# Optimization experiments

Hardware: AMD Instinct MI355X
Metric: run time of the kernel (lower is better)

The kernel has to match this reference:

```python
import jax, jax.numpy as jnp
import numpy as np

N_NODES = 50000
N_EDGES = 1600000
IN_DIM, HIDDEN, OUT_DIM = 128, 128, 64


def setup_inputs() -> dict:
    key = jax.random.key(0)
    ks = jax.random.split(key, 8)
    x = jax.random.normal(ks[0], (N_NODES, IN_DIM), dtype=jnp.float32)
    edge_index = jax.random.randint(ks[1], (2, N_EDGES), 0, N_NODES, dtype=jnp.int64)
    # SAGEConv params: lin_l applied to aggregated neighbors (with bias),
    # lin_r applied to root/self features (no bias) -- PyG defaults.
    def lin_init(k, fan_in, fan_out):
        bound = 1.0 / np.sqrt(fan_in)
        return jax.random.uniform(k, (fan_in, fan_out), jnp.float32, -bound, bound)
    W1_l = lin_init(ks[2], IN_DIM, HIDDEN)
    W1_r = lin_init(ks[3], IN_DIM, HIDDEN)
    b1 = jnp.zeros((HIDDEN,), jnp.float32)
    W2_l = lin_init(ks[4], HIDDEN, OUT_DIM)
    W2_r = lin_init(ks[5], HIDDEN, OUT_DIM)
    b2 = jnp.zeros((OUT_DIM,), jnp.float32)
    return {"x": x, "edge_index": edge_index, "W1_l": W1_l, "W1_r": W1_r,
            "b1": b1, "W2_l": W2_l, "W2_r": W2_r, "b2": b2}


def _sage_conv(h, src, dst, n_nodes, W_l, W_r, b):
    # gather messages from source nodes, mean-aggregate at destinations
    msg = h[src]                                              # [E, D]
    agg_sum = jax.ops.segment_sum(msg, dst, num_segments=n_nodes)
    deg = jax.ops.segment_sum(jnp.ones((src.shape[0],), h.dtype), dst,
                              num_segments=n_nodes)
    agg_mean = agg_sum / jnp.maximum(deg, 1.0)[:, None]       # [N, D]
    return agg_mean @ W_l + h @ W_r + b


def reference(x, edge_index, W1_l, W1_r, b1, W2_l, W2_r, b2):
    n = x.shape[0]
    src, dst = edge_index[0], edge_index[1]
    h = jax.nn.relu(_sage_conv(x, src, dst, n, W1_l, W1_r, b1))
    return _sage_conv(h, src, dst, n, W2_l, W2_r, b2)
```

## Files before the change

### kernel.cpp

```cpp
#include <hip/hip_runtime.h>

#define NN 50000
#define NE 1600000
#define BSTRIDE 96
#define BNODES 25
#define C_BKT 2000
#define P1_BLKS 256
#define P1_CHUNK 6250
#define ZID 50000
#define XCVT_BLKS 1563
#define WCVT_BLKS 48
#define PP_PREP (XCVT_BLKS + WCVT_BLKS)
#define RGRP 3128

typedef __bf16 bf16x8 __attribute__((ext_vector_type(8)));
typedef float  f32x4  __attribute__((ext_vector_type(4)));
typedef float  f32x2  __attribute__((ext_vector_type(2)));

__device__ __forceinline__ float bfLo(uint u) { union { uint i; float f; } v; v.i = u << 16; return v.f; }
__device__ __forceinline__ float bfHi(uint u) { union { uint i; float f; } v; v.i = u & 0xffff0000u; return v.f; }
__device__ __forceinline__ f32x2 bfPair(uint u) {
    union { uint i[2]; f32x2 f; } v; v.i[0] = u << 16; v.i[1] = u & 0xffff0000u; return v.f;
}
__device__ __forceinline__ ushort f2bf(float f) {
    union { float f; uint i; } v; v.f = f;
    uint r = v.i + 0x7fffu + ((v.i >> 16) & 1u);
    return (ushort)(r >> 16);
}
__device__ __forceinline__ uint pack2(float a, float b) {
    return (uint)f2bf(a) | ((uint)f2bf(b) << 16);
}
__device__ __forceinline__ bf16x8 load8(const ushort* p) {
    union { uint4 u; bf16x8 b; } v; v.u = *(const uint4*)p; return v.b;
}

#define ACC8P(u) { b0 += bfPair(u.x); b1 += bfPair(u.y); b2 += bfPair(u.z); b3 += bfPair(u.w); }

#define CVA(u, o) { f32x2 p0 = __builtin_amdgcn_cvt_pk_f32_fp8((int)(u), 0); \
                    f32x2 p1 = __builtin_amdgcn_cvt_pk_f32_fp8((int)(u), 1); \
                    a[(o)] += p0; a[(o)+1] += p1; }
#define ACCF8(v) { CVA((v).x, 0); CVA((v).y, 2); CVA((v).z, 4); CVA((v).w, 6); }

__device__ __forceinline__ int pkOff(int n, int k) {
    return (((n >> 4) * 4 + (k >> 5)) * 512) + (((k >> 3) & 3) * 128) + ((n & 15) * 8) + (k & 7);
}

__global__ __launch_bounds__(1024) void k_pp(
    const float4* __restrict__ x, ushort* __restrict__ xbp, uint* __restrict__ xf8,
    const float* __restrict__ W1l, const float* __restrict__ W1r,
    const float* __restrict__ W2l, const float* __restrict__ W2r,
    ushort* __restrict__ T1l, ushort* __restrict__ T1r,
    ushort* __restrict__ T2l, ushort* __restrict__ T2r,
    const int* __restrict__ src, const int* __restrict__ dst,
    uint* __restrict__ cells, uint* __restrict__ offc, ushort* __restrict__ hW) {
    __shared__ uint hist[C_BKT + 1];
    __shared__ uint part[250];
    const int b = blockIdx.x;
    const int tid = threadIdx.x;
    if (b < XCVT_BLKS) {
        int i = b * 1024 + tid;
        if (i < NN * 128 / 4) {
            float4 v = x[i];
            int r = i >> 5, k0 = (i & 31) * 4;
            ushort4 o; o.x = f2bf(v.x); o.y = f2bf(v.y); o.z = f2bf(v.z); o.w = f2bf(v.w);
            *(ushort4*)(xbp + pkOff(r, k0)) = o;
            uint rr = (uint)__builtin_amdgcn_cvt_pk_fp8_f32(v.x, v.y, 0, 0);
            rr = (uint)__builtin_amdgcn_cvt_pk_fp8_f32(v.z, v.w, (int)rr, 1);
            xf8[i] = rr;
        } else if (b == XCVT_BLKS - 1) {
            if (tid >= 512 && tid < 544) xf8[(size_t)ZID * 32 + (tid - 512)] = 0;
            else if (tid >= 544 && tid < 576) ((uint*)hW)[(size_t)ZID * 32 + (tid - 544)] = 0;
        }
    } else if (b < PP_PREP) {
        int i = (b - XCVT_BLKS) * 1024 + tid;
        if (i < 16384) {
            int k = i >> 7, n = i & 127; T1l[pkOff(n, k)] = f2bf(W1l[i]);
        } else if (i < 32768) {
            int j = i - 16384; int k = j >> 7, n = j & 127; T1r[pkOff(n, k)] = f2bf(W1r[j]);
        } else if (i < 40960) {
            int j = i - 32768; int k = j >> 6, n = j & 63;  T2l[pkOff(n, k)] = f2bf(W2l[j]);
        } else {
            int j = i - 40960; int k = j >> 6, n = j & 63;  T2r[pkOff(n, k)] = f2bf(W2r[j]);
        }
    } else {
        const int b2 = b - PP_PREP;
        for (int i = tid; i < C_BKT; i += 1024) hist[i] = 0;
        __syncthreads();
        const int beg = b2 * P1_CHUNK;
        for (int i = beg + tid; i < beg + P1_CHUNK; i += 1024)
            atomicAdd(&hist[dst[i] / BNODES], 1);
        __syncthreads();
        if (tid < 250) {
            uint s = 0;
            #pragma unroll
            for (int k = 0; k < 8; k++) {
                uint t = hist[tid * 8 + k];
                hist[tid * 8 + k] = s;
                s += t;
            }
            part[tid] = s;
        }
        __syncthreads();
        if (tid == 0) {
            uint run = 0;
            for (int t = 0; t < 250; t++) { uint tmp = part[t]; part[t] = run; run += tmp; }
        }
        __syncthreads();
        if (tid < 250) {
            uint bs = part[tid];
            if (bs) {
                #pragma unroll
                for (int k = 0; k < 8; k++) hist[tid * 8 + k] += bs;
            }
        }
        __syncthreads();
        for (int c = tid; c < C_BKT; c += 1024) {
            uint st = hist[c];
            uint en = (c == C_BKT - 1) ? (uint)P1_CHUNK : hist[c + 1];
            offc[(size_t)c * P1_BLKS + b2] = st | ((en - st) << 16);
        }
        __syncthreads();
        uint* myCells = cells + (size_t)b2 * P1_CHUNK;
        for (int i = beg + tid; i < beg + P1_CHUNK; i += 1024) {
            int d = dst[i];
            int s = src[i];
            int c = d / BNODES;
            uint p = atomicAdd(&hist[c], 1);
            myCells[p] = ((uint)(d - c * BNODES) << 16) | (uint)s;
        }
    }
}

__global__ __launch_bounds__(256) void k_pagg(
    const uint* __restrict__ cells, const uint* __restrict__ offc,
    const uchar* __restrict__ xf8, ushort* __restrict__ col,
    int* __restrict__ deg, ushort* __restrict__ aggp) {
    __shared__ uint hist[BNODES];
    __shared__ __align__(16) ushort colS[BNODES * BSTRIDE];
    const int bid = blockIdx.x;
    const int c = (bid & 7) * 250 + (bid >> 3);
    const int tid = threadIdx.x;
    if (tid < BNODES) hist[tid] = 0;
    __syncthreads();
    {
        uint v = offc[(size_t)c * P1_BLKS + tid];
        int st = (int)(v & 0xFFFF), n = (int)(v >> 16);
        const uint* cell = cells + (size_t)tid * P1_CHUNK + st;
        for (int j = 0; j < n; j++) {
            uint e = cell[j];
            int dl = e >> 16;
            uint p = atomicAdd(&hist[dl], 1);
            if (p < BSTRIDE) colS[dl * BSTRIDE + p] = (ushort)(e & 0xFFFF);
        }
    }
    __syncthreads();
    const int nodeBase = c * BNODES;
    if (tid < BNODES) {
        deg[nodeBase + tid] = (int)hist[tid];
        int dd = min((int)hist[tid], BSTRIDE);
        int dr = (dd + 7) & ~7;
        for (int j = dd; j < dr; j++) colS[tid * BSTRIDE + j] = (ushort)ZID;
    }
    __syncthreads();
    {
        uint4* cg = (uint4*)(col + (size_t)nodeBase * BSTRIDE);
        const uint4* cs = (const uint4*)colS;
        for (int i = tid; i < BNODES * BSTRIDE / 8; i += 256) cg[i] = cs[i];
    }
    const int wave = tid >> 6, lane = tid & 63;
    const int q = lane >> 3;
    const int cc = lane & 7;
    for (int ln = wave; ln < BNODES; ln += 4) {
        int d = (int)hist[ln];
        int dd = min(d, BSTRIDE);
        int nb = ((dd + 7) & ~7) >> 3;
        const int base = ln * BSTRIDE;
        f32x2 a[8];
        #pragma unroll
        for (int i = 0; i < 8; i++) a[i] = (f32x2){0.f, 0.f};
        int t = 0;
        for (; t + 4 <= nb; t += 4) {
            int s0 = (int)colS[base + t * 8 + q];
            int s1 = (int)colS[base + t * 8 + 8 + q];
            int s2 = (int)colS[base + t * 8 + 16 + q];
            int s3 = (int)colS[base + t * 8 + 24 + q];
            uint4 u0 = *(const uint4*)(xf8 + (size_t)s0 * 128 + cc * 16);
            uint4 u1 = *(const uint4*)(xf8 + (size_t)s1 * 128 + cc * 16);
            uint4 u2 = *(const uint4*)(xf8 + (size_t)s2 * 128 + cc * 16);
            uint4 u3 = *(const uint4*)(xf8 + (size_t)s3 * 128 + cc * 16);
            ACCF8(u0); ACCF8(u1); ACCF8(u2); ACCF8(u3);
        }
        for (; t < nb; t++) {
            int s = (int)colS[base + t * 8 + q];
            uint4 u = *(const uint4*)(xf8 + (size_t)s * 128 + cc * 16);
            ACCF8(u);
        }
        #pragma unroll
        for (int m = 8; m < 64; m <<= 1) {
            #pragma unroll
            for (int i = 0; i < 8; i++) {
                f32x2 t2;
                t2.x = __shfl_xor(a[i].x, m);
                t2.y = __shfl_xor(a[i].y, m);
                a[i] += t2;
            }
        }
        if (q == 0) {
            int node = nodeBase + ln;
            float inv = 1.f / fmaxf((float)d, 1.f);
            #pragma unroll
            for (int i = 0; i < 8; i++) a[i] *= inv;
            int basep = ((node >> 4) * 4 + (cc >> 1)) * 512 + ((cc & 1) * 2) * 128 + (node & 15) * 8;
            uint4 o;
            o.x = pack2(a[0].x, a[0].y);
            o.y = pack2(a[1].x, a[1].y);
            o.z = pack2(a[2].x, a[2].y);
            o.w = pack2(a[3].x, a[3].y);
            *(uint4*)(aggp + basep) = o;
            o.x = pack2(a[4].x, a[4].y);
            o.y = pack2(a[5].x, a[5].y);
            o.z = pack2(a[6].x, a[6].y);
            o.w = pack2(a[7].x, a[7].y);
            *(uint4*)(aggp + basep + 128) = o;
        }
    }
}

#define PAD1 136
__global__ __launch_bounds__(256) void k_gemm12(
    const ushort* __restrict__ aggp, const ushort* __restrict__ xbp,
    const ushort* __restrict__ T1l, const ushort* __restrict__ T1r,
    const ushort* __restrict__ T2l, const ushort* __restrict__ T2r,
    const float* __restrict__ b1, const float* __restrict__ b2,
    ushort* __restrict__ hW, float* __restrict__ outp) {
    __shared__ ushort hS[2][16 * PAD1];
    const int lane = threadIdx.x & 63;
    const int wave = threadIdx.x >> 6;
    const int s = wave >> 1;
    const int ch = wave & 1;
    const int quad = lane >> 4, r16 = lane & 15;
    const int row0 = blockIdx.x * 32 + s * 16;
    const int g = blockIdx.x * 2 + s;
    ushort* myS = &hS[s][0];

    f32x4 acc[4];
    #pragma unroll
    for (int nt = 0; nt < 4; nt++) acc[nt] = (f32x4){0.f, 0.f, 0.f, 0.f};
    #pragma unroll
    for (int kt = 0; kt < 4; kt++) {
        bf16x8 aAgg = load8(aggp + (size_t)(g * 4 + kt) * 512 + lane * 8);
        bf16x8 aXb  = load8(xbp  + (size_t)(g * 4 + kt) * 512 + lane * 8);
        #pragma unroll
        for (int nt = 0; nt < 4; nt++) {
            const int tile = ((ch * 4 + nt) * 4 + kt) * 512 + lane * 8;
            acc[nt] = __builtin_amdgcn_mfma_f32_16x16x32_bf16(aAgg, load8(T1l + tile), acc[nt], 0, 0, 0);
            acc[nt] = __builtin_amdgcn_mfma_f32_16x16x32_bf16(aXb,  load8(T1r + tile), acc[nt], 0, 0, 0);
        }
    }
    #pragma unroll
    for (int nt = 0; nt < 4; nt++) {
        int cc = ch * 64 + nt * 16 + r16;
        float bv = b1[cc];
        #pragma unroll
        for (int i = 0; i < 4; i++)
            myS[(quad * 4 + i) * PAD1 + cc] = f2bf(fmaxf(acc[nt][i] + bv, 0.f));
    }
    __syncthreads();

    f32x4 acc2[2], acc3[2];
    #pragma unroll
    for (int nt = 0; nt < 2; nt++) {
        acc2[nt] = (f32x4){0.f, 0.f, 0.f, 0.f};
        acc3[nt] = (f32x4){0.f, 0.f, 0.f, 0.f};
    }
    #pragma unroll
    for (int kt = 0; kt < 4; kt++) {
        bf16x8 ah = load8(&myS[r16 * PAD1 + kt * 32 + quad * 8]);
        #pragma unroll
        for (int nt = 0; nt < 2; nt++) {
            const int tile = ((ch * 2 + nt) * 4 + kt) * 512 + lane * 8;
            acc2[nt] = __builtin_amdgcn_mfma_f32_16x16x32_bf16(ah, load8(T2l + tile), acc2[nt], 0, 0, 0);
            acc3[nt] = __builtin_amdgcn_mfma_f32_16x16x32_bf16(ah, load8(T2r + tile), acc3[nt], 0, 0, 0);
        }
    }
    #pragma unroll
    for (int nt = 0; nt < 2; nt++) {
        int cc = ch * 32 + nt * 16 + r16;
        float bv = b2[cc];
        #pragma unroll
        for (int i = 0; i < 4; i++) {
            int rr = row0 + quad * 4 + i;
            if (rr < NN) {
                hW[(size_t)rr * 64 + cc] = f2bf(acc2[nt][i]);
                outp[(size_t)rr * 64 + cc] = acc3[nt][i] + bv;
            }
        }
    }
}

__global__ __launch_bounds__(256) void k_agg64f(
    const ushort* __restrict__ hW, const ushort* __restrict__ col,
    const int* __restrict__ deg, const float* __restrict__ outp,
    float* __restrict__ out) {
    __shared__ __align__(16) ushort colB[4 * BSTRIDE];
    const int tid = threadIdx.x;
    const int node0 = blockIdx.x * 4;
    if (tid < 48) {
        const uint4* cg = (const uint4*)(col + (size_t)node0 * BSTRIDE);
        *(uint4*)&colB[tid * 8] = cg[tid];
    }
    __syncthreads();
    const int wave = tid >> 6, lane = tid & 63;
    const int node = node0 + wave;
    const int q = lane >> 3;
    const int c = lane & 7;
    const int base = wave * BSTRIDE;
    int d = deg[node];
    int dd = min(d, BSTRIDE);
    int nb = ((dd + 7) & ~7) >> 3;
    f32x2 b0 = {0.f,0.f}, b1 = {0.f,0.f}, b2 = {0.f,0.f}, b3 = {0.f,0.f};
    int t = 0;
    for (; t + 4 <= nb; t += 4) {
        int s0 = (int)colB[base + t * 8 + q];
        int s1 = (int)colB[base + t * 8 + 8 + q];
        int s2 = (int)colB[base + t * 8 + 16 + q];
        int s3 = (int)colB[base + t * 8 + 24 + q];
        uint4 u0 = *(const uint4*)(hW + (size_t)s0 * 64 + c * 8);
        uint4 u1 = *(const uint4*)(hW + (size_t)s1 * 64 + c * 8);
        uint4 u2 = *(const uint4*)(hW + (size_t)s2 * 64 + c * 8);
        uint4 u3 = *(const uint4*)(hW + (size_t)s3 * 64 + c * 8);
        ACC8P(u0); ACC8P(u1); ACC8P(u2); ACC8P(u3);
    }
    for (; t < nb; t++) {
        int s = (int)colB[base + t * 8 + q];
        uint4 u = *(const uint4*)(hW + (size_t)s * 64 + c * 8);
        ACC8P(u);
    }
    #pragma unroll
    for (int m = 8; m < 64; m <<= 1) {
        f32x2 t0, t1, t2, t3;
        t0.x = __shfl_xor(b0.x, m); t0.y = __shfl_xor(b0.y, m);
        t1.x = __shfl_xor(b1.x, m); t1.y = __shfl_xor(b1.y, m);
        t2.x = __shfl_xor(b2.x, m); t2.y = __shfl_xor(b2.y, m);
        t3.x = __shfl_xor(b3.x, m); t3.y = __shfl_xor(b3.y, m);
        b0 += t0; b1 += t1; b2 += t2; b3 += t3;
    }
    if (q == 0) {
        float inv = 1.f / fmaxf((float)d, 1.f);
        float4 p0 = *(const float4*)(outp + (size_t)node * 64 + c * 8);
        float4 p1 = *(const float4*)(outp + (size_t)node * 64 + c * 8 + 4);
        float4 o;
        o.x = b0.x * inv + p0.x; o.y = b0.y * inv + p0.y;
        o.z = b1.x * inv + p0.z; o.w = b1.y * inv + p0.w;
        *(float4*)(out + (size_t)node * 64 + c * 8) = o;
        o.x = b2.x * inv + p1.x; o.y = b2.y * inv + p1.y;
        o.z = b3.x * inv + p1.z; o.w = b3.y * inv + p1.w;
        *(float4*)(out + (size_t)node * 64 + c * 8 + 4) = o;
    }
}

extern "C" void kernel_launch(void* const* d_in, const int* in_sizes, int n_in,
                              void* d_out, int out_size, void* d_ws, size_t ws_size,
                              hipStream_t stream) {
    const float* x   = (const float*)d_in[0];
    const int*   ei  = (const int*)d_in[1];
    const float* W1l = (const float*)d_in[2];
    const float* W1r = (const float*)d_in[3];
    const float* b1  = (const float*)d_in[4];
    const float* W2l = (const float*)d_in[5];
    const float* W2r = (const float*)d_in[6];
    const float* b2  = (const float*)d_in[7];
    float* out = (float*)d_out;

    const int* src = ei;
    const int* dst = ei + NE;

    char* w = (char*)d_ws;
    ushort* col   = (ushort*)w;                  w += (size_t)NN * BSTRIDE * 2;
    int* deg      = (int*)w;                     w += (size_t)50048 * 4;
    uint* offc    = (uint*)w;                    w += (size_t)C_BKT * P1_BLKS * 4;
    ushort* xbp   = (ushort*)w;                  w += (size_t)RGRP * 2048 * 2;
    ushort* T1l   = (ushort*)w;                  w += 128 * 128 * 2;
    ushort* T1r   = (ushort*)w;                  w += 128 * 128 * 2;
    ushort* T2l   = (ushort*)w;                  w += 64 * 128 * 2;
    ushort* T2r   = (ushort*)w;                  w += 64 * 128 * 2;
    ushort* aggp  = (ushort*)w;                  w += (size_t)RGRP * 2048 * 2;
    ushort* hW    = (ushort*)w;                  w += (size_t)(NN + 16) * 64 * 2;
    float* outp   = (float*)w;                   w += (size_t)NN * 64 * 4;
    uchar* xf8    = (uchar*)w;                   w += (size_t)(NN + 16) * 128;
    uint* cells   = (uint*)w;                    w += (size_t)NE * 4;

    k_pp<<<PP_PREP + P1_BLKS, 1024, 0, stream>>>(
        (const float4*)x, xbp, (uint*)xf8, W1l, W1r, W2l, W2r,
        T1l, T1r, T2l, T2r, src, dst, cells, offc, hW);

    k_pagg<<<C_BKT, 256, 0, stream>>>(cells, offc, xf8, col, deg, aggp);

    k_gemm12<<<(NN + 31) / 32, 256, 0, stream>>>(aggp, xbp, T1l, T1r, T2l, T2r, b1, b2, hW, outp);

    k_agg64f<<<NN / 4, 256, 0, stream>>>(hW, col, deg, outp, out);
}
```

Baseline: 201.9 us.

## Split gathered feature tables into column halves to shrink per-pass working set

The fp8 input features and the bf16 layer-2 hidden features are stored as two separate column-half arrays. Both aggregation kernels launch twice as many blocks, and each block gathers only one half, with 16 edges in flight per wave instead of 8. The aim is to halve the random-gather working set per block so it fits the L2/MALL caches better, and to raise parallelism. In exchange, the edge bucketing and the column-list scan in k_pagg are repeated for both halves, and padding rounds to 16.

```diff
diff --git a/kernel.cpp b/kernel.cpp
--- a/kernel.cpp
+++ b/kernel.cpp
@@ -17,8 +17,6 @@
 typedef float  f32x4  __attribute__((ext_vector_type(4)));
 typedef float  f32x2  __attribute__((ext_vector_type(2)));
 
-__device__ __forceinline__ float bfLo(uint u) { union { uint i; float f; } v; v.i = u << 16; return v.f; }
-__device__ __forceinline__ float bfHi(uint u) { union { uint i; float f; } v; v.i = u & 0xffff0000u; return v.f; }
 __device__ __forceinline__ f32x2 bfPair(uint u) {
     union { uint i[2]; f32x2 f; } v; v.i[0] = u << 16; v.i[1] = u & 0xffff0000u; return v.f;
 }
@@ -46,13 +44,15 @@
 }
 
 __global__ __launch_bounds__(1024) void k_pp(
-    const float4* __restrict__ x, ushort* __restrict__ xbp, uint* __restrict__ xf8,
+    const float4* __restrict__ x, ushort* __restrict__ xbp,
+    uint* __restrict__ xf8lo, uint* __restrict__ xf8hi,
     const float* __restrict__ W1l, const float* __restrict__ W1r,
     const float* __restrict__ W2l, const float* __restrict__ W2r,
     ushort* __restrict__ T1l, ushort* __restrict__ T1r,
     ushort* __restrict__ T2l, ushort* __restrict__ T2r,
     const int* __restrict__ src, const int* __restrict__ dst,
-    uint* __restrict__ cells, uint* __restrict__ offc, ushort* __restrict__ hW) {
+    uint* __restrict__ cells, uint* __restrict__ offc,
+    uint* __restrict__ hWlo, uint* __restrict__ hWhi) {
     __shared__ uint hist[C_BKT + 1];
     __shared__ uint part[250];
     const int b = blockIdx.x;
@@ -61,15 +61,18 @@
         int i = b * 1024 + tid;
         if (i < NN * 128 / 4) {
             float4 v = x[i];
-            int r = i >> 5, k0 = (i & 31) * 4;
+            int r = i >> 5, j = i & 31;
             ushort4 o; o.x = f2bf(v.x); o.y = f2bf(v.y); o.z = f2bf(v.z); o.w = f2bf(v.w);
-            *(ushort4*)(xbp + pkOff(r, k0)) = o;
+            *(ushort4*)(xbp + pkOff(r, j * 4)) = o;
             uint rr = (uint)__builtin_amdgcn_cvt_pk_fp8_f32(v.x, v.y, 0, 0);
             rr = (uint)__builtin_amdgcn_cvt_pk_fp8_f32(v.z, v.w, (int)rr, 1);
-            xf8[i] = rr;
+            uint* pl = (j < 16) ? xf8lo : xf8hi;
+            pl[(size_t)r * 16 + (j & 15)] = rr;
         } else if (b == XCVT_BLKS - 1) {
-            if (tid >= 512 && tid < 544) xf8[(size_t)ZID * 32 + (tid - 512)] = 0;
-            else if (tid >= 544 && tid < 576) ((uint*)hW)[(size_t)ZID * 32 + (tid - 544)] = 0;
+            if (tid >= 512 && tid < 528) xf8lo[(size_t)ZID * 16 + (tid - 512)] = 0;
+            else if (tid >= 528 && tid < 544) xf8hi[(size_t)ZID * 16 + (tid - 528)] = 0;
+            else if (tid >= 544 && tid < 560) hWlo[(size_t)ZID * 16 + (tid - 544)] = 0;
+            else if (tid >= 560 && tid < 576) hWhi[(size_t)ZID * 16 + (tid - 560)] = 0;
         }
     } else if (b < PP_PREP) {
         int i = (b - XCVT_BLKS) * 1024 + tid;
@@ -133,13 +136,15 @@
 
 __global__ __launch_bounds__(256) void k_pagg(
     const uint* __restrict__ cells, const uint* __restrict__ offc,
-    const uchar* __restrict__ xf8, ushort* __restrict__ col,
-    int* __restrict__ deg, ushort* __restrict__ aggp) {
+    const uchar* __restrict__ xf8lo, const uchar* __restrict__ xf8hi,
+    ushort* __restrict__ col, int* __restrict__ deg, ushort* __restrict__ aggp) {
     __shared__ uint hist[BNODES];
     __shared__ __align__(16) ushort colS[BNODES * BSTRIDE];
     const int bid = blockIdx.x;
-    const int c = (bid & 7) * 250 + (bid >> 3);
+    const int h = bid & 1;
+    const int c = ((bid >> 1) & 3) * 500 + (bid >> 3);
     const int tid = threadIdx.x;
+    const uchar* xf8 = h ? xf8hi : xf8lo;
     if (tid < BNODES) hist[tid] = 0;
     __syncthreads();
     {
@@ -156,47 +161,43 @@
     __syncthreads();
     const int nodeBase = c * BNODES;
     if (tid < BNODES) {
-        deg[nodeBase + tid] = (int)hist[tid];
+        if (h == 0) deg[nodeBase + tid] = (int)hist[tid];
         int dd = min((int)hist[tid], BSTRIDE);
-        int dr = (dd + 7) & ~7;
+        int dr = (dd + 15) & ~15;
         for (int j = dd; j < dr; j++) colS[tid * BSTRIDE + j] = (ushort)ZID;
     }
     __syncthreads();
-    {
+    if (h == 0) {
         uint4* cg = (uint4*)(col + (size_t)nodeBase * BSTRIDE);
         const uint4* cs = (const uint4*)colS;
         for (int i = tid; i < BNODES * BSTRIDE / 8; i += 256) cg[i] = cs[i];
     }
     const int wave = tid >> 6, lane = tid & 63;
-    const int q = lane >> 3;
-    const int cc = lane & 7;
+    const int q = lane >> 2;
+    const int c4 = lane & 3;
     for (int ln = wave; ln < BNODES; ln += 4) {
         int d = (int)hist[ln];
         int dd = min(d, BSTRIDE);
-        int nb = ((dd + 7) & ~7) >> 3;
+        int nb = ((dd + 15) & ~15) >> 4;
         const int base = ln * BSTRIDE;
         f32x2 a[8];
         #pragma unroll
         for (int i = 0; i < 8; i++) a[i] = (f32x2){0.f, 0.f};
         int t = 0;
-        for (; t + 4 <= nb; t += 4) {
-            int s0 = (int)colS[base + t * 8 + q];
-            int s1 = (int)colS[base + t * 8 + 8 + q];
-            int s2 = (int)colS[base + t * 8 + 16 + q];
-            int s3 = (int)colS[base + t * 8 + 24 + q];
-            uint4 u0 = *(const uint4*)(xf8 + (size_t)s0 * 128 + cc * 16);
-            uint4 u1 = *(const uint4*)(xf8 + (size_t)s1 * 128 + cc * 16);
-            uint4 u2 = *(const uint4*)(xf8 + (size_t)s2 * 128 + cc * 16);
-            uint4 u3 = *(const uint4*)(xf8 + (size_t)s3 * 128 + cc * 16);
-            ACCF8(u0); ACCF8(u1); ACCF8(u2); ACCF8(u3);
+        for (; t + 2 <= nb; t += 2) {
+            int s0 = (int)colS[base + t * 16 + q];
+            int s1 = (int)colS[base + t * 16 + 16 + q];
+            uint4 u0 = *(const uint4*)(xf8 + (size_t)s0 * 64 + c4 * 16);
+            uint4 u1 = *(const uint4*)(xf8 + (size_t)s1 * 64 + c4 * 16);
+            ACCF8(u0); ACCF8(u1);
         }
         for (; t < nb; t++) {
-            int s = (int)colS[base + t * 8 + q];
-            uint4 u = *(const uint4*)(xf8 + (size_t)s * 128 + cc * 16);
+            int s = (int)colS[base + t * 16 + q];
+            uint4 u = *(const uint4*)(xf8 + (size_t)s * 64 + c4 * 16);
             ACCF8(u);
         }
         #pragma unroll
-        for (int m = 8; m < 64; m <<= 1) {
+        for (int m = 4; m < 64; m <<= 1) {
             #pragma unroll
             for (int i = 0; i < 8; i++) {
                 f32x2 t2;
@@ -210,7 +211,8 @@
             float inv = 1.f / fmaxf((float)d, 1.f);
             #pragma unroll
             for (int i = 0; i < 8; i++) a[i] *= inv;
-            int basep = ((node >> 4) * 4 + (cc >> 1)) * 512 + ((cc & 1) * 2) * 128 + (node & 15) * 8;
+            int kt = h * 2 + (c4 >> 1);
+            int basep = ((node >> 4) * 4 + kt) * 512 + ((c4 & 1) * 2) * 128 + (node & 15) * 8;
             uint4 o;
             o.x = pack2(a[0].x, a[0].y);
             o.y = pack2(a[1].x, a[1].y);
@@ -232,7 +234,7 @@
     const ushort* __restrict__ T1l, const ushort* __restrict__ T1r,
     const ushort* __restrict__ T2l, const ushort* __restrict__ T2r,
     const float* __restrict__ b1, const float* __restrict__ b2,
-    ushort* __restrict__ hW, float* __restrict__ outp) {
+    ushort* __restrict__ hWlo, ushort* __restrict__ hWhi, float* __restrict__ outp) {
     __shared__ ushort hS[2][16 * PAD1];
     const int lane = threadIdx.x & 63;
     const int wave = threadIdx.x >> 6;
@@ -283,6 +285,7 @@
             acc3[nt] = __builtin_amdgcn_mfma_f32_16x16x32_bf16(ah, load8(T2r + tile), acc3[nt], 0, 0, 0);
         }
     }
+    ushort* hWp = ch ? hWhi : hWlo;
     #pragma unroll
     for (int nt = 0; nt < 2; nt++) {
         int cc = ch * 32 + nt * 16 + r16;
@@ -291,7 +294,7 @@
         for (int i = 0; i < 4; i++) {
             int rr = row0 + quad * 4 + i;
             if (rr < NN) {
-                hW[(size_t)rr * 64 + cc] = f2bf(acc2[nt][i]);
+                hWp[(size_t)rr * 32 + nt * 16 + r16] = f2bf(acc2[nt][i]);
                 outp[(size_t)rr * 64 + cc] = acc3[nt][i] + bv;
             }
         }
@@ -299,45 +302,44 @@
 }
 
 __global__ __launch_bounds__(256) void k_agg64f(
-    const ushort* __restrict__ hW, const ushort* __restrict__ col,
-    const int* __restrict__ deg, const float* __restrict__ outp,
-    float* __restrict__ out) {
+    const ushort* __restrict__ hWlo, const ushort* __restrict__ hWhi,
+    const ushort* __restrict__ col, const int* __restrict__ deg,
+    const float* __restrict__ outp, float* __restrict__ out) {
     __shared__ __align__(16) ushort colB[4 * BSTRIDE];
+    const int bid = blockIdx.x;
+    const int h = bid & 1;
+    const int node0 = (bid >> 1) * 4;
     const int tid = threadIdx.x;
-    const int node0 = blockIdx.x * 4;
     if (tid < 48) {
         const uint4* cg = (const uint4*)(col + (size_t)node0 * BSTRIDE);
         *(uint4*)&colB[tid * 8] = cg[tid];
     }
     __syncthreads();
+    const ushort* hw = h ? hWhi : hWlo;
     const int wave = tid >> 6, lane = tid & 63;
     const int node = node0 + wave;
-    const int q = lane >> 3;
-    const int c = lane & 7;
+    const int q = lane >> 2;
+    const int c4 = lane & 3;
     const int base = wave * BSTRIDE;
     int d = deg[node];
     int dd = min(d, BSTRIDE);
-    int nb = ((dd + 7) & ~7) >> 3;
+    int nb = ((dd + 15) & ~15) >> 4;
     f32x2 b0 = {0.f,0.f}, b1 = {0.f,0.f}, b2 = {0.f,0.f}, b3 = {0.f,0.f};
     int t = 0;
-    for (; t + 4 <= nb; t += 4) {
-        int s0 = (int)colB[base + t * 8 + q];
-        int s1 = (int)colB[base + t * 8 + 8 + q];
-        int s2 = (int)colB[base + t * 8 + 16 + q];
-        int s3 = (int)colB[base + t * 8 + 24 + q];
-        uint4 u0 = *(const uint4*)(hW + (size_t)s0 * 64 + c * 8);
-        uint4 u1 = *(const uint4*)(hW + (size_t)s1 * 64 + c * 8);
-        uint4 u2 = *(const uint4*)(hW + (size_t)s2 * 64 + c * 8);
-        uint4 u3 = *(const uint4*)(hW + (size_t)s3 * 64 + c * 8);
-        ACC8P(u0); ACC8P(u1); ACC8P(u2); ACC8P(u3);
+    for (; t + 2 <= nb; t += 2) {
+        int s0 = (int)colB[base + t * 16 + q];
+        int s1 = (int)colB[base + t * 16 + 16 + q];
+        uint4 u0 = *(const uint4*)(hw + (size_t)s0 * 32 + c4 * 8);
+        uint4 u1 = *(const uint4*)(hw + (size_t)s1 * 32 + c4 * 8);
+        ACC8P(u0); ACC8P(u1);
     }
     for (; t < nb; t++) {
-        int s = (int)colB[base + t * 8 + q];
-        uint4 u = *(const uint4*)(hW + (size_t)s * 64 + c * 8);
+        int s = (int)colB[base + t * 16 + q];
+        uint4 u = *(const uint4*)(hw + (size_t)s * 32 + c4 * 8);
         ACC8P(u);
     }
     #pragma unroll
-    for (int m = 8; m < 64; m <<= 1) {
+    for (int m = 4; m < 64; m <<= 1) {
         f32x2 t0, t1, t2, t3;
         t0.x = __shfl_xor(b0.x, m); t0.y = __shfl_xor(b0.y, m);
         t1.x = __shfl_xor(b1.x, m); t1.y = __shfl_xor(b1.y, m);
@@ -347,15 +349,16 @@
     }
     if (q == 0) {
         float inv = 1.f / fmaxf((float)d, 1.f);
-        float4 p0 = *(const float4*)(outp + (size_t)node * 64 + c * 8);
-        float4 p1 = *(const float4*)(outp + (size_t)node * 64 + c * 8 + 4);
+        size_t o0 = (size_t)node * 64 + h * 32 + c4 * 8;
+        float4 p0 = *(const float4*)(outp + o0);
+        float4 p1 = *(const float4*)(outp + o0 + 4);
         float4 o;
         o.x = b0.x * inv + p0.x; o.y = b0.y * inv + p0.y;
         o.z = b1.x * inv + p0.z; o.w = b1.y * inv + p0.w;
-        *(float4*)(out + (size_t)node * 64 + c * 8) = o;
+        *(float4*)(out + o0) = o;
         o.x = b2.x * inv + p1.x; o.y = b2.y * inv + p1.y;
         o.z = b3.x * inv + p1.z; o.w = b3.y * inv + p1.w;
-        *(float4*)(out + (size_t)node * 64 + c * 8 + 4) = o;
+        *(float4*)(out + o0 + 4) = o;
     }
 }
 
@@ -385,18 +388,20 @@
     ushort* T2l   = (ushort*)w;                  w += 64 * 128 * 2;
     ushort* T2r   = (ushort*)w;                  w += 64 * 128 * 2;
     ushort* aggp  = (ushort*)w;                  w += (size_t)RGRP * 2048 * 2;
-    ushort* hW    = (ushort*)w;                  w += (size_t)(NN + 16) * 64 * 2;
+    ushort* hWlo  = (ushort*)w;                  w += (size_t)(NN + 16) * 32 * 2;
+    ushort* hWhi  = (ushort*)w;                  w += (size_t)(NN + 16) * 32 * 2;
     float* outp   = (float*)w;                   w += (size_t)NN * 64 * 4;
-    uchar* xf8    = (uchar*)w;                   w += (size_t)(NN + 16) * 128;
+    uchar* xf8lo  = (uchar*)w;                   w += (size_t)(NN + 16) * 64;
+    uchar* xf8hi  = (uchar*)w;                   w += (size_t)(NN + 16) * 64;
     uint* cells   = (uint*)w;                    w += (size_t)NE * 4;
 
     k_pp<<<PP_PREP + P1_BLKS, 1024, 0, stream>>>(
-        (const float4*)x, xbp, (uint*)xf8, W1l, W1r, W2l, W2r,
-        T1l, T1r, T2l, T2r, src, dst, cells, offc, hW);
-
-    k_pagg<<<C_BKT, 256, 0, stream>>>(cells, offc, xf8, col, deg, aggp);
-
-    k_gemm12<<<(NN + 31) / 32, 256, 0, stream>>>(aggp, xbp, T1l, T1r, T2l, T2r, b1, b2, hW, outp);
-
-    k_agg64f<<<NN / 4, 256, 0, stream>>>(hW, col, deg, outp, out);
-}
+        (const float4*)x, xbp, (uint*)xf8lo, (uint*)xf8hi, W1l, W1r, W2l, W2r,
+        T1l, T1r, T2l, T2r, src, dst, cells, offc, (uint*)hWlo, (uint*)hWhi);
+
+    k_pagg<<<C_BKT * 2, 256, 0, stream>>>(cells, offc, xf8lo, xf8hi, col, deg, aggp);
+
+    k_gemm12<<<(NN + 31) / 32, 256, 0, stream>>>(aggp, xbp, T1l, T1r, T2l, T2r, b1, b2, hWlo, hWhi, outp);
+
+    k_agg64f<<<(NN / 4) * 2, 256, 0, stream>>>(hWlo, hWhi, col, deg, outp, out);
+}
```

Result: slower. 258.8 us (+28.2%).

## Replace two-pass bucketed CSR build with direct global-atomic scatter into padded adjacency

Applied to the files above, without the earlier changes.

Drops the per-block shared-memory histogram, prefix scan and bucketed cells staging. Each edge now takes a slot with a global atomicAdd on a per-node counter and writes its source straight into the fixed-stride column array. This needs a separate zeroing kernel, and the counters double as degrees. The layer-1 aggregation now reads the prebuilt columns per node and handles the partial last group by masking lanes to the zero row instead of padding. This removes a full extra pass over the edges, but adds contention from 1.6M global atomics and scattered 2-byte writes, and the neighbor order within each node becomes nondeterministic.

```diff
diff --git a/kernel.cpp b/kernel.cpp
--- a/kernel.cpp
+++ b/kernel.cpp
@@ -3,11 +3,9 @@
 #define NN 50000
 #define NE 1600000
 #define BSTRIDE 96
-#define BNODES 25
-#define C_BKT 2000
-#define P1_BLKS 256
-#define P1_CHUNK 6250
 #define ZID 50000
+#define SCAT_BLKS 256
+#define SCHUNK 6250
 #define XCVT_BLKS 1563
 #define WCVT_BLKS 48
 #define PP_PREP (XCVT_BLKS + WCVT_BLKS)
@@ -17,8 +15,6 @@
 typedef float  f32x4  __attribute__((ext_vector_type(4)));
 typedef float  f32x2  __attribute__((ext_vector_type(2)));
 
-__device__ __forceinline__ float bfLo(uint u) { union { uint i; float f; } v; v.i = u << 16; return v.f; }
-__device__ __forceinline__ float bfHi(uint u) { union { uint i; float f; } v; v.i = u & 0xffff0000u; return v.f; }
 __device__ __forceinline__ f32x2 bfPair(uint u) {
     union { uint i[2]; f32x2 f; } v; v.i[0] = u << 16; v.i[1] = u & 0xffff0000u; return v.f;
 }
@@ -43,6 +39,11 @@
 
 __device__ __forceinline__ int pkOff(int n, int k) {
     return (((n >> 4) * 4 + (k >> 5)) * 512) + (((k >> 3) & 3) * 128) + ((n & 15) * 8) + (k & 7);
+}
+
+__global__ __launch_bounds__(256) void k_zero(int* __restrict__ cur) {
+    int i = blockIdx.x * 256 + threadIdx.x;
+    if (i < NN) cur[i] = 0;
 }
 
 __global__ __launch_bounds__(1024) void k_pp(
@@ -52,18 +53,16 @@
     ushort* __restrict__ T1l, ushort* __restrict__ T1r,
     ushort* __restrict__ T2l, ushort* __restrict__ T2r,
     const int* __restrict__ src, const int* __restrict__ dst,
-    uint* __restrict__ cells, uint* __restrict__ offc, ushort* __restrict__ hW) {
-    __shared__ uint hist[C_BKT + 1];
-    __shared__ uint part[250];
+    int* __restrict__ cur, ushort* __restrict__ col, ushort* __restrict__ hW) {
     const int b = blockIdx.x;
     const int tid = threadIdx.x;
     if (b < XCVT_BLKS) {
         int i = b * 1024 + tid;
         if (i < NN * 128 / 4) {
             float4 v = x[i];
-            int r = i >> 5, k0 = (i & 31) * 4;
+            int r = i >> 5, j = i & 31;
             ushort4 o; o.x = f2bf(v.x); o.y = f2bf(v.y); o.z = f2bf(v.z); o.w = f2bf(v.w);
-            *(ushort4*)(xbp + pkOff(r, k0)) = o;
+            *(ushort4*)(xbp + pkOff(r, j * 4)) = o;
             uint rr = (uint)__builtin_amdgcn_cvt_pk_fp8_f32(v.x, v.y, 0, 0);
             rr = (uint)__builtin_amdgcn_cvt_pk_fp8_f32(v.z, v.w, (int)rr, 1);
             xf8[i] = rr;
@@ -84,145 +83,88 @@
         }
     } else {
         const int b2 = b - PP_PREP;
-        for (int i = tid; i < C_BKT; i += 1024) hist[i] = 0;
-        __syncthreads();
-        const int beg = b2 * P1_CHUNK;
-        for (int i = beg + tid; i < beg + P1_CHUNK; i += 1024)
-            atomicAdd(&hist[dst[i] / BNODES], 1);
-        __syncthreads();
-        if (tid < 250) {
-            uint s = 0;
-            #pragma unroll
-            for (int k = 0; k < 8; k++) {
-                uint t = hist[tid * 8 + k];
-                hist[tid * 8 + k] = s;
-                s += t;
-            }
-            part[tid] = s;
-        }
-        __syncthreads();
-        if (tid == 0) {
-            uint run = 0;
-            for (int t = 0; t < 250; t++) { uint tmp = part[t]; part[t] = run; run += tmp; }
-        }
-        __syncthreads();
-        if (tid < 250) {
-            uint bs = part[tid];
-            if (bs) {
-                #pragma unroll
-                for (int k = 0; k < 8; k++) hist[tid * 8 + k] += bs;
-            }
-        }
-        __syncthreads();
-        for (int c = tid; c < C_BKT; c += 1024) {
-            uint st = hist[c];
-            uint en = (c == C_BKT - 1) ? (uint)P1_CHUNK : hist[c + 1];
-            offc[(size_t)c * P1_BLKS + b2] = st | ((en - st) << 16);
-        }
-        __syncthreads();
-        uint* myCells = cells + (size_t)b2 * P1_CHUNK;
-        for (int i = beg + tid; i < beg + P1_CHUNK; i += 1024) {
+        const int beg = b2 * SCHUNK;
+        for (int i = beg + tid; i < beg + SCHUNK; i += 1024) {
             int d = dst[i];
             int s = src[i];
-            int c = d / BNODES;
-            uint p = atomicAdd(&hist[c], 1);
-            myCells[p] = ((uint)(d - c * BNODES) << 16) | (uint)s;
+            uint p = (uint)atomicAdd(&cur[d], 1);
+            if (p < BSTRIDE) col[(size_t)d * BSTRIDE + p] = (ushort)s;
         }
     }
 }
 
 __global__ __launch_bounds__(256) void k_pagg(
-    const uint* __restrict__ cells, const uint* __restrict__ offc,
-    const uchar* __restrict__ xf8, ushort* __restrict__ col,
-    int* __restrict__ deg, ushort* __restrict__ aggp) {
-    __shared__ uint hist[BNODES];
-    __shared__ __align__(16) ushort colS[BNODES * BSTRIDE];
-    const int bid = blockIdx.x;
-    const int c = (bid & 7) * 250 + (bid >> 3);
+    const uchar* __restrict__ xf8, const ushort* __restrict__ col,
+    const int* __restrict__ deg, ushort* __restrict__ aggp) {
+    __shared__ __align__(16) ushort colB[4 * BSTRIDE];
     const int tid = threadIdx.x;
-    if (tid < BNODES) hist[tid] = 0;
+    const int node0 = blockIdx.x * 4;
+    if (tid < 48) {
+        const uint4* cg = (const uint4*)(col + (size_t)node0 * BSTRIDE);
+        *(uint4*)&colB[tid * 8] = cg[tid];
+    }
     __syncthreads();
-    {
-        uint v = offc[(size_t)c * P1_BLKS + tid];
-        int st = (int)(v & 0xFFFF), n = (int)(v >> 16);
-        const uint* cell = cells + (size_t)tid * P1_CHUNK + st;
-        for (int j = 0; j < n; j++) {
-            uint e = cell[j];
-            int dl = e >> 16;
-            uint p = atomicAdd(&hist[dl], 1);
-            if (p < BSTRIDE) colS[dl * BSTRIDE + p] = (ushort)(e & 0xFFFF);
-        }
-    }
-    __syncthreads();
-    const int nodeBase = c * BNODES;
-    if (tid < BNODES) {
-        deg[nodeBase + tid] = (int)hist[tid];
-        int dd = min((int)hist[tid], BSTRIDE);
-        int dr = (dd + 7) & ~7;
-        for (int j = dd; j < dr; j++) colS[tid * BSTRIDE + j] = (ushort)ZID;
-    }
-    __syncthreads();
-    {
-        uint4* cg = (uint4*)(col + (size_t)nodeBase * BSTRIDE);
-        const uint4* cs = (const uint4*)colS;
-        for (int i = tid; i < BNODES * BSTRIDE / 8; i += 256) cg[i] = cs[i];
-    }
     const int wave = tid >> 6, lane = tid & 63;
+    const int node = node0 + wave;
     const int q = lane >> 3;
-    const int cc = lane & 7;
-    for (int ln = wave; ln < BNODES; ln += 4) {
-        int d = (int)hist[ln];
-        int dd = min(d, BSTRIDE);
-        int nb = ((dd + 7) & ~7) >> 3;
-        const int base = ln * BSTRIDE;
-        f32x2 a[8];
-        #pragma unroll
-        for (int i = 0; i < 8; i++) a[i] = (f32x2){0.f, 0.f};
-        int t = 0;
-        for (; t + 4 <= nb; t += 4) {
-            int s0 = (int)colS[base + t * 8 + q];
-            int s1 = (int)colS[base + t * 8 + 8 + q];
-            int s2 = (int)colS[base + t * 8 + 16 + q];
-            int s3 = (int)colS[base + t * 8 + 24 + q];
-            uint4 u0 = *(const uint4*)(xf8 + (size_t)s0 * 128 + cc * 16);
-            uint4 u1 = *(const uint4*)(xf8 + (size_t)s1 * 128 + cc * 16);
-            uint4 u2 = *(const uint4*)(xf8 + (size_t)s2 * 128 + cc * 16);
-            uint4 u3 = *(const uint4*)(xf8 + (size_t)s3 * 128 + cc * 16);
-            ACCF8(u0); ACCF8(u1); ACCF8(u2); ACCF8(u3);
-        }
-        for (; t < nb; t++) {
-            int s = (int)colS[base + t * 8 + q];
-            uint4 u = *(const uint4*)(xf8 + (size_t)s * 128 + cc * 16);
-            ACCF8(u);
-        }
-        #pragma unroll
-        for (int m = 8; m < 64; m <<= 1) {
-            #pragma unroll
-            for (int i = 0; i < 8; i++) {
-                f32x2 t2;
-                t2.x = __shfl_xor(a[i].x, m);
-                t2.y = __shfl_xor(a[i].y, m);
-                a[i] += t2;
-            }
-        }
-        if (q == 0) {
-            int node = nodeBase + ln;
-            float inv = 1.f / fmaxf((float)d, 1.f);
-            #pragma unroll
-            for (int i = 0; i < 8; i++) a[i] *= inv;
-            int basep = ((node >> 4) * 4 + (cc >> 1)) * 512 + ((cc & 1) * 2) * 128 + (node & 15) * 8;
-            uint4 o;
-            o.x = pack2(a[0].x, a[0].y);
-            o.y = pack2(a[1].x, a[1].y);
-            o.z = pack2(a[2].x, a[2].y);
-            o.w = pack2(a[3].x, a[3].y);
-            *(uint4*)(aggp + basep) = o;
-            o.x = pack2(a[4].x, a[4].y);
-            o.y = pack2(a[5].x, a[5].y);
-            o.z = pack2(a[6].x, a[6].y);
-            o.w = pack2(a[7].x, a[7].y);
-            *(uint4*)(aggp + basep + 128) = o;
-        }
+    const int c = lane & 7;
+    const int base = wave * BSTRIDE;
+    int d = deg[node];
+    int dd = min(d, BSTRIDE);
+    int nf = dd >> 3;
+    int rem = dd & 7;
+    f32x2 a[8];
+    #pragma unroll
+    for (int i = 0; i < 8; i++) a[i] = (f32x2){0.f, 0.f};
+    int t = 0;
+    for (; t + 4 <= nf; t += 4) {
+        int s0 = (int)colB[base + t * 8 + q];
+        int s1 = (int)colB[base + t * 8 + 8 + q];
+        int s2 = (int)colB[base + t * 8 + 16 + q];
+        int s3 = (int)colB[base + t * 8 + 24 + q];
+        uint4 u0 = *(const uint4*)(xf8 + (size_t)s0 * 128 + c * 16);
+        uint4 u1 = *(const uint4*)(xf8 + (size_t)s1 * 128 + c * 16);
+        uint4 u2 = *(const uint4*)(xf8 + (size_t)s2 * 128 + c * 16);
+        uint4 u3 = *(const uint4*)(xf8 + (size_t)s3 * 128 + c * 16);
+        ACCF8(u0); ACCF8(u1); ACCF8(u2); ACCF8(u3);
+    }
+    for (; t < nf; t++) {
+        int s = (int)colB[base + t * 8 + q];
+        uint4 u = *(const uint4*)(xf8 + (size_t)s * 128 + c * 16);
+        ACCF8(u);
+    }
+    if (rem) {
+        int slot = nf * 8 + q;
+        int s = (slot < dd) ? (int)colB[base + slot] : ZID;
+        uint4 u = *(const uint4*)(xf8 + (size_t)s * 128 + c * 16);
+        ACCF8(u);
+    }
+    #pragma unroll
+    for (int m = 8; m < 64; m <<= 1) {
+        #pragma unroll
+        for (int i = 0; i < 8; i++) {
+            f32x2 t2;
+            t2.x = __shfl_xor(a[i].x, m);
+            t2.y = __shfl_xor(a[i].y, m);
+            a[i] += t2;
+        }
+    }
+    if (q == 0) {
+        float inv = 1.f / fmaxf((float)d, 1.f);
+        #pragma unroll
+        for (int i = 0; i < 8; i++) a[i] *= inv;
+        int basep = ((node >> 4) * 4 + (c >> 1)) * 512 + ((c & 1) * 2) * 128 + (node & 15) * 8;
+        uint4 o;
+        o.x = pack2(a[0].x, a[0].y);
+        o.y = pack2(a[1].x, a[1].y);
+        o.z = pack2(a[2].x, a[2].y);
+        o.w = pack2(a[3].x, a[3].y);
+        *(uint4*)(aggp + basep) = o;
+        o.x = pack2(a[4].x, a[4].y);
+        o.y = pack2(a[5].x, a[5].y);
+        o.z = pack2(a[6].x, a[6].y);
+        o.w = pack2(a[7].x, a[7].y);
+        *(uint4*)(aggp + basep + 128) = o;
     }
 }
 
@@ -317,10 +259,11 @@
     const int base = wave * BSTRIDE;
     int d = deg[node];
     int dd = min(d, BSTRIDE);
-    int nb = ((dd + 7) & ~7) >> 3;
+    int nf = dd >> 3;
+    int rem = dd & 7;
     f32x2 b0 = {0.f,0.f}, b1 = {0.f,0.f}, b2 = {0.f,0.f}, b3 = {0.f,0.f};
     int t = 0;
-    for (; t + 4 <= nb; t += 4) {
+    for (; t + 4 <= nf; t += 4) {
         int s0 = (int)colB[base + t * 8 + q];
         int s1 = (int)colB[base + t * 8 + 8 + q];
         int s2 = (int)colB[base + t * 8 + 16 + q];
@@ -331,8 +274,14 @@
         uint4 u3 = *(const uint4*)(hW + (size_t)s3 * 64 + c * 8);
         ACC8P(u0); ACC8P(u1); ACC8P(u2); ACC8P(u3);
     }
-    for (; t < nb; t++) {
+    for (; t < nf; t++) {
         int s = (int)colB[base + t * 8 + q];
+        uint4 u = *(const uint4*)(hW + (size_t)s * 64 + c * 8);
+        ACC8P(u);
+    }
+    if (rem) {
+        int slot = nf * 8 + q;
+        int s = (slot < dd) ? (int)colB[base + slot] : ZID;
         uint4 u = *(const uint4*)(hW + (size_t)s * 64 + c * 8);
         ACC8P(u);
     }
@@ -377,8 +326,7 @@
 
     char* w = (char*)d_ws;
     ushort* col   = (ushort*)w;                  w += (size_t)NN * BSTRIDE * 2;
-    int* deg      = (int*)w;                     w += (size_t)50048 * 4;
-    uint* offc    = (uint*)w;                    w += (size_t)C_BKT * P1_BLKS * 4;
+    int* cur      = (int*)w;                     w += (size_t)50048 * 4;
     ushort* xbp   = (ushort*)w;                  w += (size_t)RGRP * 2048 * 2;
     ushort* T1l   = (ushort*)w;                  w += 128 * 128 * 2;
     ushort* T1r   = (ushort*)w;                  w += 128 * 128 * 2;
@@ -388,15 +336,16 @@
     ushort* hW    = (ushort*)w;                  w += (size_t)(NN + 16) * 64 * 2;
     float* outp   = (float*)w;                   w += (size_t)NN * 64 * 4;
     uchar* xf8    = (uchar*)w;                   w += (size_t)(NN + 16) * 128;
-    uint* cells   = (uint*)w;                    w += (size_t)NE * 4;
-
-    k_pp<<<PP_PREP + P1_BLKS, 1024, 0, stream>>>(
+
+    k_zero<<<(NN + 255) / 256, 256, 0, stream>>>(cur);
+
+    k_pp<<<PP_PREP + SCAT_BLKS, 1024, 0, stream>>>(
         (const float4*)x, xbp, (uint*)xf8, W1l, W1r, W2l, W2r,
-        T1l, T1r, T2l, T2r, src, dst, cells, offc, hW);
-
-    k_pagg<<<C_BKT, 256, 0, stream>>>(cells, offc, xf8, col, deg, aggp);
+        T1l, T1r, T2l, T2r, src, dst, cur, col, hW);
+
+    k_pagg<<<NN / 4, 256, 0, stream>>>(xf8, col, cur, aggp);
 
     k_gemm12<<<(NN + 31) / 32, 256, 0, stream>>>(aggp, xbp, T1l, T1r, T2l, T2r, b1, b2, hW, outp);
 
-    k_agg64f<<<NN / 4, 256, 0, stream>>>(hW, col, deg, outp, out);
-}
+    k_agg64f<<<NN / 4, 256, 0, stream>>>(hW, col, cur, outp, out);
+}
```

After: 279.3 us. +38.3%, slower.

## Split bucket slotting from first-layer gather into separate kernels

Applied to the files above, without the earlier changes.

The fused kernel that built each bucket's neighbor lists and then gathered FP8 features is split in two. The new k_slot kernel handles only slotting, with 50-node buckets, 512 threads and two threads per partition. A new k_gath1 kernel then aggregates one node per wave across many small blocks, and both gathers handle the partial last group of 8 neighbors with a masked load instead of relying on padding. This is meant to raise parallelism and balance load in the first aggregation, at the cost of an extra launch and a round trip of the col array through global memory.

```diff
diff --git a/kernel.cpp b/kernel.cpp
--- a/kernel.cpp
+++ b/kernel.cpp
@@ -3,8 +3,8 @@
 #define NN 50000
 #define NE 1600000
 #define BSTRIDE 96
-#define BNODES 25
-#define C_BKT 2000
+#define BNODES 50
+#define C_BKT 1000
 #define P1_BLKS 256
 #define P1_CHUNK 6250
 #define ZID 50000
@@ -17,8 +17,6 @@
 typedef float  f32x4  __attribute__((ext_vector_type(4)));
 typedef float  f32x2  __attribute__((ext_vector_type(2)));
 
-__device__ __forceinline__ float bfLo(uint u) { union { uint i; float f; } v; v.i = u << 16; return v.f; }
-__device__ __forceinline__ float bfHi(uint u) { union { uint i; float f; } v; v.i = u & 0xffff0000u; return v.f; }
 __device__ __forceinline__ f32x2 bfPair(uint u) {
     union { uint i[2]; f32x2 f; } v; v.i[0] = u << 16; v.i[1] = u & 0xffff0000u; return v.f;
 }
@@ -54,16 +52,16 @@
     const int* __restrict__ src, const int* __restrict__ dst,
     uint* __restrict__ cells, uint* __restrict__ offc, ushort* __restrict__ hW) {
     __shared__ uint hist[C_BKT + 1];
-    __shared__ uint part[250];
+    __shared__ uint part[128];
     const int b = blockIdx.x;
     const int tid = threadIdx.x;
     if (b < XCVT_BLKS) {
         int i = b * 1024 + tid;
         if (i < NN * 128 / 4) {
             float4 v = x[i];
-            int r = i >> 5, k0 = (i & 31) * 4;
+            int r = i >> 5, j = i & 31;
             ushort4 o; o.x = f2bf(v.x); o.y = f2bf(v.y); o.z = f2bf(v.z); o.w = f2bf(v.w);
-            *(ushort4*)(xbp + pkOff(r, k0)) = o;
+            *(ushort4*)(xbp + pkOff(r, j * 4)) = o;
             uint rr = (uint)__builtin_amdgcn_cvt_pk_fp8_f32(v.x, v.y, 0, 0);
             rr = (uint)__builtin_amdgcn_cvt_pk_fp8_f32(v.z, v.w, (int)rr, 1);
             xf8[i] = rr;
@@ -90,7 +88,7 @@
         for (int i = beg + tid; i < beg + P1_CHUNK; i += 1024)
             atomicAdd(&hist[dst[i] / BNODES], 1);
         __syncthreads();
-        if (tid < 250) {
+        if (tid < 125) {
             uint s = 0;
             #pragma unroll
             for (int k = 0; k < 8; k++) {
@@ -103,10 +101,10 @@
         __syncthreads();
         if (tid == 0) {
             uint run = 0;
-            for (int t = 0; t < 250; t++) { uint tmp = part[t]; part[t] = run; run += tmp; }
-        }
-        __syncthreads();
-        if (tid < 250) {
+            for (int t = 0; t < 125; t++) { uint tmp = part[t]; part[t] = run; run += tmp; }
+        }
+        __syncthreads();
+        if (tid < 125) {
             uint bs = part[tid];
             if (bs) {
                 #pragma unroll
@@ -131,22 +129,22 @@
     }
 }
 
-__global__ __launch_bounds__(256) void k_pagg(
+__global__ __launch_bounds__(512) void k_slot(
     const uint* __restrict__ cells, const uint* __restrict__ offc,
-    const uchar* __restrict__ xf8, ushort* __restrict__ col,
-    int* __restrict__ deg, ushort* __restrict__ aggp) {
+    ushort* __restrict__ col, int* __restrict__ deg) {
     __shared__ uint hist[BNODES];
     __shared__ __align__(16) ushort colS[BNODES * BSTRIDE];
     const int bid = blockIdx.x;
-    const int c = (bid & 7) * 250 + (bid >> 3);
+    const int c = (bid & 7) * 125 + (bid >> 3);
     const int tid = threadIdx.x;
     if (tid < BNODES) hist[tid] = 0;
     __syncthreads();
     {
-        uint v = offc[(size_t)c * P1_BLKS + tid];
+        const int b = tid >> 1, sub = tid & 1;
+        uint v = offc[(size_t)c * P1_BLKS + b];
         int st = (int)(v & 0xFFFF), n = (int)(v >> 16);
-        const uint* cell = cells + (size_t)tid * P1_CHUNK + st;
-        for (int j = 0; j < n; j++) {
+        const uint* cell = cells + (size_t)b * P1_CHUNK + st;
+        for (int j = sub; j < n; j += 2) {
             uint e = cell[j];
             int dl = e >> 16;
             uint p = atomicAdd(&hist[dl], 1);
@@ -165,64 +163,82 @@
     {
         uint4* cg = (uint4*)(col + (size_t)nodeBase * BSTRIDE);
         const uint4* cs = (const uint4*)colS;
-        for (int i = tid; i < BNODES * BSTRIDE / 8; i += 256) cg[i] = cs[i];
-    }
+        for (int i = tid; i < BNODES * BSTRIDE / 8; i += 512) cg[i] = cs[i];
+    }
+}
+
+__global__ __launch_bounds__(256) void k_gath1(
+    const uchar* __restrict__ xf8, const ushort* __restrict__ col,
+    const int* __restrict__ deg, ushort* __restrict__ aggp) {
+    __shared__ __align__(16) ushort colB[4 * BSTRIDE];
+    const int tid = threadIdx.x;
+    const int node0 = blockIdx.x * 4;
+    if (tid < 48) {
+        const uint4* cg = (const uint4*)(col + (size_t)node0 * BSTRIDE);
+        *(uint4*)&colB[tid * 8] = cg[tid];
+    }
+    __syncthreads();
     const int wave = tid >> 6, lane = tid & 63;
+    const int node = node0 + wave;
     const int q = lane >> 3;
-    const int cc = lane & 7;
-    for (int ln = wave; ln < BNODES; ln += 4) {
-        int d = (int)hist[ln];
-        int dd = min(d, BSTRIDE);
-        int nb = ((dd + 7) & ~7) >> 3;
-        const int base = ln * BSTRIDE;
-        f32x2 a[8];
-        #pragma unroll
-        for (int i = 0; i < 8; i++) a[i] = (f32x2){0.f, 0.f};
-        int t = 0;
-        for (; t + 4 <= nb; t += 4) {
-            int s0 = (int)colS[base + t * 8 + q];
-            int s1 = (int)colS[base + t * 8 + 8 + q];
-            int s2 = (int)colS[base + t * 8 + 16 + q];
-            int s3 = (int)colS[base + t * 8 + 24 + q];
-            uint4 u0 = *(const uint4*)(xf8 + (size_t)s0 * 128 + cc * 16);
-            uint4 u1 = *(const uint4*)(xf8 + (size_t)s1 * 128 + cc * 16);
-            uint4 u2 = *(const uint4*)(xf8 + (size_t)s2 * 128 + cc * 16);
-            uint4 u3 = *(const uint4*)(xf8 + (size_t)s3 * 128 + cc * 16);
-            ACCF8(u0); ACCF8(u1); ACCF8(u2); ACCF8(u3);
-        }
-        for (; t < nb; t++) {
-            int s = (int)colS[base + t * 8 + q];
-            uint4 u = *(const uint4*)(xf8 + (size_t)s * 128 + cc * 16);
-            ACCF8(u);
-        }
-        #pragma unroll
-        for (int m = 8; m < 64; m <<= 1) {
-            #pragma unroll
-            for (int i = 0; i < 8; i++) {
-                f32x2 t2;
-                t2.x = __shfl_xor(a[i].x, m);
-                t2.y = __shfl_xor(a[i].y, m);
-                a[i] += t2;
-            }
-        }
-        if (q == 0) {
-            int node = nodeBase + ln;
-            float inv = 1.f / fmaxf((float)d, 1.f);
-            #pragma unroll
-            for (int i = 0; i < 8; i++) a[i] *= inv;
-            int basep = ((node >> 4) * 4 + (cc >> 1)) * 512 + ((cc & 1) * 2) * 128 + (node & 15) * 8;
-            uint4 o;
-            o.x = pack2(a[0].x, a[0].y);
-            o.y = pack2(a[1].x, a[1].y);
-            o.z = pack2(a[2].x, a[2].y);
-            o.w = pack2(a[3].x, a[3].y);
-            *(uint4*)(aggp + basep) = o;
-            o.x = pack2(a[4].x, a[4].y);
-            o.y = pack2(a[5].x, a[5].y);
-            o.z = pack2(a[6].x, a[6].y);
-            o.w = pack2(a[7].x, a[7].y);
-            *(uint4*)(aggp + basep + 128) = o;
-        }
+    const int c = lane & 7;
+    const int base = wave * BSTRIDE;
+    int d = deg[node];
+    int dd = min(d, BSTRIDE);
+    int nf = dd >> 3;
+    int rem = dd & 7;
+    f32x2 a[8];
+    #pragma unroll
+    for (int i = 0; i < 8; i++) a[i] = (f32x2){0.f, 0.f};
+    int t = 0;
+    for (; t + 4 <= nf; t += 4) {
+        int s0 = (int)colB[base + t * 8 + q];
+        int s1 = (int)colB[base + t * 8 + 8 + q];
+        int s2 = (int)colB[base + t * 8 + 16 + q];
+        int s3 = (int)colB[base + t * 8 + 24 + q];
+        uint4 u0 = *(const uint4*)(xf8 + (size_t)s0 * 128 + c * 16);
+        uint4 u1 = *(const uint4*)(xf8 + (size_t)s1 * 128 + c * 16);
+        uint4 u2 = *(const uint4*)(xf8 + (size_t)s2 * 128 + c * 16);
+        uint4 u3 = *(const uint4*)(xf8 + (size_t)s3 * 128 + c * 16);
+        ACCF8(u0); ACCF8(u1); ACCF8(u2); ACCF8(u3);
+    }
+    for (; t < nf; t++) {
+        int s = (int)colB[base + t * 8 + q];
+        uint4 u = *(const uint4*)(xf8 + (size_t)s * 128 + c * 16);
+        ACCF8(u);
+    }
+    if (rem) {
+        int slot = nf * 8 + q;
+        int s = (slot < dd) ? (int)colB[base + slot] : ZID;
+        uint4 u = *(const uint4*)(xf8 + (size_t)s * 128 + c * 16);
+        ACCF8(u);
+    }
+    #pragma unroll
+    for (int m = 8; m < 64; m <<= 1) {
+        #pragma unroll
+        for (int i = 0; i < 8; i++) {
+            f32x2 t2;
+            t2.x = __shfl_xor(a[i].x, m);
+            t2.y = __shfl_xor(a[i].y, m);
+            a[i] += t2;
+        }
+    }
+    if (q == 0) {
+        float inv = 1.f / fmaxf((float)d, 1.f);
+        #pragma unroll
+        for (int i = 0; i < 8; i++) a[i] *= inv;
+        int basep = ((node >> 4) * 4 + (c >> 1)) * 512 + ((c & 1) * 2) * 128 + (node & 15) * 8;
+        uint4 o;
+        o.x = pack2(a[0].x, a[0].y);
+        o.y = pack2(a[1].x, a[1].y);
+        o.z = pack2(a[2].x, a[2].y);
+        o.w = pack2(a[3].x, a[3].y);
+        *(uint4*)(aggp + basep) = o;
+        o.x = pack2(a[4].x, a[4].y);
+        o.y = pack2(a[5].x, a[5].y);
+        o.z = pack2(a[6].x, a[6].y);
+        o.w = pack2(a[7].x, a[7].y);
+        *(uint4*)(aggp + basep + 128) = o;
     }
 }
 
@@ -317,10 +333,11 @@
     const int base = wave * BSTRIDE;
     int d = deg[node];
     int dd = min(d, BSTRIDE);
-    int nb = ((dd + 7) & ~7) >> 3;
+    int nf = dd >> 3;
+    int rem = dd & 7;
     f32x2 b0 = {0.f,0.f}, b1 = {0.f,0.f}, b2 = {0.f,0.f}, b3 = {0.f,0.f};
     int t = 0;
-    for (; t + 4 <= nb; t += 4) {
+    for (; t + 4 <= nf; t += 4) {
         int s0 = (int)colB[base + t * 8 + q];
         int s1 = (int)colB[base + t * 8 + 8 + q];
         int s2 = (int)colB[base + t * 8 + 16 + q];
@@ -331,8 +348,14 @@
         uint4 u3 = *(const uint4*)(hW + (size_t)s3 * 64 + c * 8);
         ACC8P(u0); ACC8P(u1); ACC8P(u2); ACC8P(u3);
     }
-    for (; t < nb; t++) {
+    for (; t < nf; t++) {
         int s = (int)colB[base + t * 8 + q];
+        uint4 u = *(const uint4*)(hW + (size_t)s * 64 + c * 8);
+        ACC8P(u);
+    }
+    if (rem) {
+        int slot = nf * 8 + q;
+        int s = (slot < dd) ? (int)colB[base + slot] : ZID;
         uint4 u = *(const uint4*)(hW + (size_t)s * 64 + c * 8);
         ACC8P(u);
     }
@@ -394,7 +417,9 @@
         (const float4*)x, xbp, (uint*)xf8, W1l, W1r, W2l, W2r,
         T1l, T1r, T2l, T2r, src, dst, cells, offc, hW);
 
-    k_pagg<<<C_BKT, 256, 0, stream>>>(cells, offc, xf8, col, deg, aggp);
+    k_slot<<<C_BKT, 512, 0, stream>>>(cells, offc, col, deg);
+
+    k_gath1<<<NN / 4, 256, 0, stream>>>(xf8, col, deg, aggp);
 
     k_gemm12<<<(NN + 31) / 32, 256, 0, stream>>>(aggp, xbp, T1l, T1r, T2l, T2r, b1, b2, hW, outp);
 
```

Measured after the change: 202.8 us. About the same (+0.5%).
